# Optimization experiments

Measured on AMD Instinct MI355X. Metric: run time of the kernel, lower is better.

## Reference

```python
import jax, jax.numpy as jnp
import numpy as np

N, E = 50000, 800000
F_IN, HID, HEADS, NCLS = 128, 64, 4, 16
NEG_SLOPE = 0.2


def setup_inputs() -> dict:
    key = jax.random.key(0)
    ks = jax.random.split(key, 16)
    def glorot(k, shape):
        fan_in, fan_out = shape[0], shape[-1]
        lim = jnp.sqrt(6.0 / (fan_in + fan_out))
        return jax.random.uniform(k, shape, jnp.float32, -lim, lim)
    x = jax.random.normal(ks[0], (N, F_IN), jnp.float32)
    edge_index = jax.random.randint(ks[1], (2, E), 0, N, dtype=jnp.int64)
    inp = {"x": x, "edge_index": edge_index}
    # layer 1: F_IN -> HID x HEADS (concat)
    inp["W1"] = glorot(ks[2], (F_IN, HEADS * HID))
    inp["a1_src"] = glorot(ks[3], (HEADS, HID))
    inp["a1_dst"] = glorot(ks[4], (HEADS, HID))
    inp["b1"] = jnp.zeros((HEADS * HID,), jnp.float32)
    # layer 2: HEADS*HID -> HID x HEADS (concat)
    inp["W2"] = glorot(ks[5], (HEADS * HID, HEADS * HID))
    inp["a2_src"] = glorot(ks[6], (HEADS, HID))
    inp["a2_dst"] = glorot(ks[7], (HEADS, HID))
    inp["b2"] = jnp.zeros((HEADS * HID,), jnp.float32)
    # layer 3: HEADS*HID -> NCLS, heads=1, concat=False (mean)
    inp["W3"] = glorot(ks[8], (HEADS * HID, NCLS))
    inp["a3_src"] = glorot(ks[9], (1, NCLS))
    inp["a3_dst"] = glorot(ks[10], (1, NCLS))
    inp["b3"] = jnp.zeros((NCLS,), jnp.float32)
    return inp


def gat_conv(x, src, dst, W, a_src, a_dst, b, heads, out_dim, concat):
    n = x.shape[0]
    h = (x @ W).reshape(n, heads, out_dim)           # [N, H, D]
    s_src = jnp.sum(h * a_src, axis=-1)              # [N, H]
    s_dst = jnp.sum(h * a_dst, axis=-1)              # [N, H]
    e = jax.nn.leaky_relu(s_src[src] + s_dst[dst], NEG_SLOPE)  # [E, H]
    # segment softmax over incoming edges of each dst node
    m = jax.ops.segment_max(e, dst, num_segments=n)
    ex = jnp.exp(e - m[dst])
    z = jax.ops.segment_sum(ex, dst, num_segments=n)
    alpha = ex / z[dst]                              # [E, H]
    msg = h[src] * alpha[:, :, None]                 # [E, H, D]
    out = jax.ops.segment_sum(msg, dst, num_segments=n)  # [N, H, D]
    out = out.reshape(n, heads * out_dim) if concat else out.mean(axis=1)
    return out + b


def reference(x, edge_index, W1, a1_src, a1_dst, b1, W2, a2_src, a2_dst, b2,
              W3, a3_src, a3_dst, b3):
    n = x.shape[0]
    loop = jnp.arange(n, dtype=edge_index.dtype)
    src = jnp.concatenate([edge_index[0], loop])     # add self-loops (PyG default)
    dst = jnp.concatenate([edge_index[1], loop])
    h = jax.nn.elu(gat_conv(x, src, dst, W1, a1_src, a1_dst, b1, HEADS, HID, True))
    h = jax.nn.elu(gat_conv(h, src, dst, W2, a2_src, a2_dst, b2, HEADS, HID, True))
    h = gat_conv(h, src, dst, W3, a3_src, a3_dst, b3, 1, NCLS, False)
    return jax.nn.log_softmax(h, axis=1)
```

## Files before the change

kernel.cpp:

```cpp
#include <hip/hip_runtime.h>
#include <hip/hip_bf16.h>
#include <math.h>

#define N_NODES 50000
#define N_EDGES 800000
#define F_IN    128
#define HID     64
#define HEADS   4
#define NCLS    16
#define NEG_SLOPE 0.2f

typedef __attribute__((ext_vector_type(8))) _Float16 half8v;
typedef __attribute__((ext_vector_type(4))) float f32x4;
typedef __attribute__((ext_vector_type(2))) float f32x2;

static __device__ __forceinline__ float lrelu(float x) {
    return x >= 0.f ? x : NEG_SLOPE * x;
}
static __device__ __forceinline__ unsigned short f2h(float f) {
    _Float16 h = (_Float16)f;
    return __builtin_bit_cast(unsigned short, h);
}
static __device__ __forceinline__ float h2f(unsigned short u) {
    return (float)__builtin_bit_cast(_Float16, u);
}

__global__ void k_zero(int4* __restrict__ p, int n4) {
    int i = blockIdx.x * blockDim.x + threadIdx.x;
    if (i < n4) p[i] = int4{0, 0, 0, 0};
}

#define NB_WT1  128
#define NB_WT2  256
#define NB_HIST 3125
__global__ void k_prep(const float* __restrict__ W1, unsigned short* __restrict__ W1t,
                       const float* __restrict__ W2, unsigned short* __restrict__ W2t,
                       const int* __restrict__ dst, int* __restrict__ counts,
                       unsigned short* __restrict__ rank) {
    int bid = blockIdx.x, tid = threadIdx.x;
    if (bid < NB_WT1) {
        int i = bid * 256 + tid;
        int k = i >> 8, c = i & 255;
        W1t[c * F_IN + k] = f2h(W1[i]);
    } else if (bid < NB_WT1 + NB_WT2) {
        int i = (bid - NB_WT1) * 256 + tid;
        int k = i >> 8, c = i & 255;
        W2t[c * 256 + k] = f2h(W2[i]);
    } else {
        int i = (bid - NB_WT1 - NB_WT2) * 256 + tid;
        if (i < N_EDGES) rank[i] = (unsigned short)atomicAdd(&counts[dst[i]], 1);
    }
}

__global__ __launch_bounds__(256) void k_scan1(const int* __restrict__ counts, int* __restrict__ incl,
                                               int* __restrict__ bsums, int n) {
    __shared__ int wsum[4];
    int blk = blockIdx.x, tid = threadIdx.x;
    int lane = tid & 63, w = tid >> 6;
    int i0 = blk * 1024 + tid * 4;
    int v[4];
    #pragma unroll
    for (int j = 0; j < 4; j++) v[j] = (i0 + j < n) ? counts[i0 + j] : 0;
    int t = v[0] + v[1] + v[2] + v[3];
    int x = t;
    #pragma unroll
    for (int d = 1; d < 64; d <<= 1) { int y = __shfl_up(x, d); if (lane >= d) x += y; }
    if (lane == 63) wsum[w] = x;
    __syncthreads();
    int woff = 0;
    #pragma unroll
    for (int ww = 0; ww < 4; ww++) woff += (ww < w) ? wsum[ww] : 0;
    int p = woff + x - t;
    #pragma unroll
    for (int j = 0; j < 4; j++) { p += v[j]; if (i0 + j < n) incl[i0 + j] = p; }
    if (tid == 255) bsums[blk] = woff + x;
}

__global__ void k_scan2(const int* __restrict__ bsums, int* __restrict__ boffs, int nb, int* rowptr_end) {
    int lane = threadIdx.x;
    int v = (lane < nb) ? bsums[lane] : 0;
    int x = v;
    #pragma unroll
    for (int d = 1; d < 64; d <<= 1) { int y = __shfl_up(x, d); if (lane >= d) x += y; }
    if (lane < nb) boffs[lane] = x - v;
    if (lane == 63) *rowptr_end = x;
}

__global__ void k_scan3(const int* __restrict__ incl, const int* __restrict__ counts,
                        const int* __restrict__ boffs, int* __restrict__ rowptr, int n) {
    int i = blockIdx.x * blockDim.x + threadIdx.x;
    if (i < n) rowptr[i] = boffs[i >> 10] + incl[i] - counts[i];
}

static __device__ __forceinline__ int swz(int r, int lc) {
    return r * 4 + (lc ^ (r & 3) ^ ((r >> 2) & 1));
}

template<int CONVA>
static __device__ __forceinline__ void gemm_body(
        int bid, const void* __restrict__ Av, const unsigned short* __restrict__ Bt,
        const float* __restrict__ asrc, const float* __restrict__ adst,
        unsigned char* __restrict__ C8, float* __restrict__ s_src, float* __restrict__ s_dst,
        int M, int K, unsigned short* Asm, unsigned short* Bsm) {
    int tid = threadIdx.x;
    int lane = tid & 63, wid = tid >> 6;
    int bx = bid & 1, by = bid >> 1;
    int row0 = by * 128, col0 = bx * 128;
    int wr = wid >> 1, wc = wid & 1;
    f32x4 acc[4][4] = {};

    for (int k0 = 0; k0 < K; k0 += 32) {
        __syncthreads();
        #pragma unroll
        for (int s = 0; s < 2; s++) {
            int c = tid + s * 256;
            int row = c >> 2, lc = c & 3;
            int gr = row0 + row; if (gr >= M) gr = 0;
            uint4 va;
            if (CONVA) {
                const float* Af = (const float*)Av + (size_t)gr * K + k0 + lc * 8;
                float4 fa = *(const float4*)Af;
                float4 fb = *(const float4*)(Af + 4);
                va.x = (unsigned)f2h(fa.x) | ((unsigned)f2h(fa.y) << 16);
                va.y = (unsigned)f2h(fa.z) | ((unsigned)f2h(fa.w) << 16);
                va.z = (unsigned)f2h(fb.x) | ((unsigned)f2h(fb.y) << 16);
                va.w = (unsigned)f2h(fb.z) | ((unsigned)f2h(fb.w) << 16);
            } else {
                va = *(const uint4*)((const unsigned short*)Av + (size_t)gr * K + k0 + lc * 8);
            }
            *(uint4*)(&Asm[swz(row, lc) * 8]) = va;
            uint4 vb = *(const uint4*)(Bt + (size_t)(col0 + row) * K + k0 + lc * 8);
            *(uint4*)(&Bsm[swz(row, lc) * 8]) = vb;
        }
        __syncthreads();
        half8v af[4], bg[4];
        int lq = lane >> 4;
        #pragma unroll
        for (int m = 0; m < 4; m++) {
            int r = wr * 64 + m * 16 + (lane & 15);
            af[m] = *(const half8v*)(&Asm[swz(r, lq) * 8]);
        }
        #pragma unroll
        for (int n = 0; n < 4; n++) {
            int r = wc * 64 + n * 16 + (lane & 15);
            bg[n] = *(const half8v*)(&Bsm[swz(r, lq) * 8]);
        }
        #pragma unroll
        for (int m = 0; m < 4; m++)
            #pragma unroll
            for (int n = 0; n < 4; n++)
                acc[m][n] = __builtin_amdgcn_mfma_f32_16x16x32_f16(af[m], bg[n], acc[m][n], 0, 0, 0);
    }

    #pragma unroll
    for (int m = 0; m < 4; m++) {
        #pragma unroll
        for (int r = 0; r < 4; r++) {
            int row = row0 + wr * 64 + m * 16 + (lane >> 4) * 4 + r;
            if (row < M) {
                int q01 = __builtin_amdgcn_cvt_pk_fp8_f32(acc[m][0][r], acc[m][1][r], 0, false);
                int q23 = __builtin_amdgcn_cvt_pk_fp8_f32(acc[m][2][r], acc[m][3][r], 0, false);
                size_t base = (size_t)row * 256 + col0 + wc * 64 + (lane & 15);
                C8[base]      = (unsigned char)(q01 & 0xff);
                C8[base + 16] = (unsigned char)((q01 >> 8) & 0xff);
                C8[base + 32] = (unsigned char)(q23 & 0xff);
                C8[base + 48] = (unsigned char)((q23 >> 8) & 0xff);
            }
        }
    }

    int c16 = lane & 15, lq = lane >> 4;
    int head = bx * 2 + wc;
    float avs[4], avd[4];
    #pragma unroll
    for (int nn = 0; nn < 4; nn++) {
        avs[nn] = asrc[head * 64 + nn * 16 + c16];
        avd[nn] = adst[head * 64 + nn * 16 + c16];
    }
    #pragma unroll
    for (int mm = 0; mm < 4; mm++) {
        #pragma unroll
        for (int r = 0; r < 4; r++) {
            float ps = 0.f, pd = 0.f;
            #pragma unroll
            for (int nn = 0; nn < 4; nn++) {
                ps += acc[mm][nn][r] * avs[nn];
                pd += acc[mm][nn][r] * avd[nn];
            }
            #pragma unroll
            for (int off = 1; off < 16; off <<= 1) {
                ps += __shfl_xor(ps, off);
                pd += __shfl_xor(pd, off);
            }
            if (c16 == 0) {
                int grow = row0 + wr * 64 + mm * 16 + lq * 4 + r;
                if (grow < M) {
                    s_src[grow * 4 + head] = ps;
                    s_dst[grow * 4 + head] = pd;
                }
            }
        }
    }
}

__global__ __launch_bounds__(256) void k_gemm_mfma(const unsigned short* __restrict__ A,
                                                   const unsigned short* __restrict__ Bt,
                                                   const float* __restrict__ asrc,
                                                   const float* __restrict__ adst,
                                                   unsigned char* __restrict__ C8,
                                                   float* __restrict__ s_src,
                                                   float* __restrict__ s_dst,
                                                   int M, int K) {
    __shared__ unsigned short Asm[128 * 32];
    __shared__ unsigned short Bsm[128 * 32];
    gemm_body<0>(blockIdx.x, A, Bt, asrc, adst, C8, s_src, s_dst, M, K, Asm, Bsm);
}

__global__ __launch_bounds__(256) void k_b(const float* __restrict__ A,
                                           const unsigned short* __restrict__ Bt,
                                           const float* __restrict__ asrc,
                                           const float* __restrict__ adst,
                                           unsigned char* __restrict__ C8,
                                           float* __restrict__ s_src,
                                           float* __restrict__ s_dst,
                                           int M, int K, int gemmBlocks,
                                           const int* __restrict__ src, const int* __restrict__ dst,
                                           const int* __restrict__ rowptr,
                                           const unsigned short* __restrict__ rank,
                                           unsigned short* __restrict__ col, int e) {
    __shared__ unsigned short Asm[128 * 32];
    __shared__ unsigned short Bsm[128 * 32];
    int bid = blockIdx.x;
    if (bid < gemmBlocks) {
        gemm_body<1>(bid, A, Bt, asrc, adst, C8, s_src, s_dst, M, K, Asm, Bsm);
    } else {
        int half = (e + 1) >> 1;
        int i = (bid - gemmBlocks) * 256 + (int)threadIdx.x;
        if (i < half) {
            int d = dst[i];
            col[rowptr[d] + rank[i]] = (unsigned short)src[i];
        }
        int j = i + half;
        if (j < e) {
            int d = dst[j];
            col[rowptr[d] + rank[j]] = (unsigned short)src[j];
        }
    }
}

__global__ void k_aggregate(const unsigned char* __restrict__ h8, const int* __restrict__ rowptr,
                            const unsigned short* __restrict__ col,
                            const float* __restrict__ s_src, const float* __restrict__ s_dst,
                            const float* __restrict__ bias,
                            unsigned short* __restrict__ out, int n) {
    int wave = (blockIdx.x * blockDim.x + threadIdx.x) >> 6;
    int lane = threadIdx.x & 63;
    int half = lane >> 5, l5 = lane & 31;
    int node = wave * 2 + half;
    if (node >= n) return;
    int head = l5 >> 3;
    int j8 = l5 & 7;
    int base8 = lane & ~7;
    unsigned foff = (unsigned)(l5 * 8);
    int rs = rowptr[node], re = rowptr[node + 1];
    float sd = s_dst[node * 4 + head];

    float z = 0.f;
    f32x2 a01 = {0.f, 0.f}, a23 = {0.f, 0.f}, a45 = {0.f, 0.f}, a67 = {0.f, 0.f};
    #define PEDGE(SV) __expf(fminf(lrelu((SV) + sd), 80.f))
    #define ACC8(P, HV) { \
        f32x2 pbc = {(P), (P)}; \
        f32x2 v0 = __builtin_amdgcn_cvt_pk_f32_fp8((HV).x, false); \
        f32x2 v1 = __builtin_amdgcn_cvt_pk_f32_fp8((HV).x, true);  \
        f32x2 v2 = __builtin_amdgcn_cvt_pk_f32_fp8((HV).y, false); \
        f32x2 v3 = __builtin_amdgcn_cvt_pk_f32_fp8((HV).y, true);  \
        asm("v_pk_fma_f32 %0, %1, %2, %0" : "+v"(a01) : "v"(v0), "v"(pbc)); \
        asm("v_pk_fma_f32 %0, %1, %2, %0" : "+v"(a23) : "v"(v1), "v"(pbc)); \
        asm("v_pk_fma_f32 %0, %1, %2, %0" : "+v"(a45) : "v"(v2), "v"(pbc)); \
        asm("v_pk_fma_f32 %0, %1, %2, %0" : "+v"(a67) : "v"(v3), "v"(pbc)); \
        z += (P); }

    {
        float pself = PEDGE(s_src[node * 4 + head]);
        uint2 own = *(const uint2*)(h8 + (((unsigned)node << 8) + foff));
        ACC8(pself, own);
    }
    int i = rs;
    for (; i + 7 < re; i += 8) {
        unsigned cc[8];
        #pragma unroll
        for (int j = 0; j < 8; j++) cc[j] = col[i + j];
        float s_own = s_src[cc[j8] * 4 + head];
        uint2 hv[8];
        #pragma unroll
        for (int j = 0; j < 8; j++)
            hv[j] = *(const uint2*)(h8 + ((cc[j] << 8) + foff));
        float p_own = PEDGE(s_own);
        float pv[8];
        #pragma unroll
        for (int j = 0; j < 8; j++) pv[j] = __shfl(p_own, base8 + j);
        #pragma unroll
        for (int j = 0; j < 8; j++) { ACC8(pv[j], hv[j]); }
    }
    for (; i + 3 < re; i += 4) {
        unsigned cc[4];
        #pragma unroll
        for (int j = 0; j < 4; j++) cc[j] = col[i + j];
        float s_own = s_src[cc[j8 & 3] * 4 + head];
        uint2 hv[4];
        #pragma unroll
        for (int j = 0; j < 4; j++)
            hv[j] = *(const uint2*)(h8 + ((cc[j] << 8) + foff));
        float p_own = PEDGE(s_own);
        float pv[4];
        #pragma unroll
        for (int j = 0; j < 4; j++) pv[j] = __shfl(p_own, base8 + j);
        #pragma unroll
        for (int j = 0; j < 4; j++) { ACC8(pv[j], hv[j]); }
    }
    for (; i < re; i++) {
        unsigned c0 = col[i];
        float s0 = s_src[c0 * 4 + head];
        uint2 h0 = *(const uint2*)(h8 + ((c0 << 8) + foff));
        float p0 = PEDGE(s0);
        ACC8(p0, h0);
    }
    #undef ACC8
    #undef PEDGE

    float inv = 1.f / z;
    int f0 = l5 * 8;
    float4 bv0 = *(const float4*)(bias + f0);
    float4 bv1 = *(const float4*)(bias + f0 + 4);
    float o[8];
    o[0] = a01.x * inv + bv0.x; o[1] = a01.y * inv + bv0.y;
    o[2] = a23.x * inv + bv0.z; o[3] = a23.y * inv + bv0.w;
    o[4] = a45.x * inv + bv1.x; o[5] = a45.y * inv + bv1.y;
    o[6] = a67.x * inv + bv1.z; o[7] = a67.y * inv + bv1.w;
    #pragma unroll
    for (int j = 0; j < 8; j++) o[j] = o[j] > 0.f ? o[j] : __expf(o[j]) - 1.f;
    uint4 ov;
    unsigned* w = (unsigned*)&ov;
    #pragma unroll
    for (int j = 0; j < 4; j++)
        w[j] = (unsigned)f2h(o[2 * j]) | ((unsigned)f2h(o[2 * j + 1]) << 16);
    *(uint4*)(out + (size_t)node * 256 + f0) = ov;
}

__global__ __launch_bounds__(256) void k_gemm3(const unsigned short* __restrict__ A,
                                               const float* __restrict__ B,
                                               const float* __restrict__ a3s,
                                               const float* __restrict__ a3d,
                                               unsigned short* __restrict__ C,
                                               float* __restrict__ s_src,
                                               float* __restrict__ s_dst,
                                               int M, int K) {
    __shared__ float Bs[256 * 16];
    for (int i = threadIdx.x; i < K * 16; i += 256) Bs[i] = B[i];
    __syncthreads();
    int tx = threadIdx.x & 15;
    int ty = threadIdx.x >> 4;
    int row = blockIdx.x * 16 + ty;
    if (row >= M) return;
    const unsigned short* Ar = A + (size_t)row * K;
    float acc = 0.f;
    for (int kk = 0; kk < K; kk += 8) {
        uint4 va = *(const uint4*)(Ar + kk);
        const unsigned* u = (const unsigned*)&va;
        #pragma unroll
        for (int j = 0; j < 4; j++) {
            float lo = h2f((unsigned short)(u[j] & 0xffff));
            float hi = h2f((unsigned short)(u[j] >> 16));
            acc += lo * Bs[(kk + 2 * j) * 16 + tx] + hi * Bs[(kk + 2 * j + 1) * 16 + tx];
        }
    }
    C[(size_t)row * 16 + tx] = f2h(acc);
    float ps = acc * a3s[tx], pd = acc * a3d[tx];
    #pragma unroll
    for (int off = 1; off < 16; off <<= 1) {
        ps += __shfl_xor(ps, off);
        pd += __shfl_xor(pd, off);
    }
    if (tx == 0) { s_src[row] = ps; s_dst[row] = pd; }
}

__global__ void k_agg3(const unsigned short* __restrict__ h3, const int* __restrict__ rowptr,
                       const unsigned short* __restrict__ col,
                       const float* __restrict__ s_src, const float* __restrict__ s_dst,
                       const float* __restrict__ b3,
                       float* __restrict__ outp, int n) {
    int wave = (blockIdx.x * blockDim.x + threadIdx.x) >> 6;
    int lane = threadIdx.x & 63;
    if (wave >= n) return;
    int g = lane >> 4, c = lane & 15;
    int gbase = lane & ~15;
    int rs = rowptr[wave], re = rowptr[wave + 1];
    float sdn = s_dst[wave];

    float z = 0.f, acc = 0.f;
    if (g == 0) {
        float p = __expf(fminf(lrelu(s_src[wave] + sdn), 80.f));
        z += p;
        acc += p * h2f(h3[(size_t)wave * 16 + c]);
    }
    int i = rs + g;
    for (; i + 12 < re; i += 16) {
        int ss[4];
        #pragma unroll
        for (int j = 0; j < 4; j++) ss[j] = col[i + 4 * j];
        float q_own = s_src[ss[c & 3]];
        float v0 = h2f(h3[(size_t)ss[0] * 16 + c]), v1 = h2f(h3[(size_t)ss[1] * 16 + c]);
        float v2 = h2f(h3[(size_t)ss[2] * 16 + c]), v3 = h2f(h3[(size_t)ss[3] * 16 + c]);
        float p_own = __expf(fminf(lrelu(q_own + sdn), 80.f));
        float p0 = __shfl(p_own, gbase + 0);
        float p1 = __shfl(p_own, gbase + 1);
        float p2 = __shfl(p_own, gbase + 2);
        float p3 = __shfl(p_own, gbase + 3);
        z += (p0 + p1) + (p2 + p3);
        acc += p0 * v0 + p1 * v1 + p2 * v2 + p3 * v3;
    }
    for (; i < re; i += 4) {
        int s = col[i];
        float p = __expf(fminf(lrelu(s_src[s] + sdn), 80.f));
        z += p;
        acc += p * h2f(h3[(size_t)s * 16 + c]);
    }
    z += __shfl_xor(z, 16);  z += __shfl_xor(z, 32);
    acc += __shfl_xor(acc, 16); acc += __shfl_xor(acc, 32);
    if (lane < 16) {
        float v = acc / z + b3[c];
        float mm = v;
        #pragma unroll
        for (int off = 1; off < 16; off <<= 1) mm = fmaxf(mm, __shfl_xor(mm, off));
        float se = __expf(v - mm);
        #pragma unroll
        for (int off = 1; off < 16; off <<= 1) se += __shfl_xor(se, off);
        outp[(size_t)wave * 16 + c] = v - mm - logf(se);
    }
}

extern "C" void kernel_launch(void* const* d_in, const int* in_sizes, int n_in,
                              void* d_out, int out_size, void* d_ws, size_t ws_size,
                              hipStream_t stream) {
    const float* x      = (const float*)d_in[0];
    const int*   ei     = (const int*)d_in[1];
    const float* W1     = (const float*)d_in[2];
    const float* a1_src = (const float*)d_in[3];
    const float* a1_dst = (const float*)d_in[4];
    const float* b1     = (const float*)d_in[5];
    const float* W2     = (const float*)d_in[6];
    const float* a2_src = (const float*)d_in[7];
    const float* a2_dst = (const float*)d_in[8];
    const float* b2     = (const float*)d_in[9];
    const float* W3     = (const float*)d_in[10];
    const float* a3_src = (const float*)d_in[11];
    const float* a3_dst = (const float*)d_in[12];
    const float* b3     = (const float*)d_in[13];
    float* outp = (float*)d_out;

    const int N = N_NODES, E = N_EDGES;
    const int* src = ei;
    const int* dst = ei + E;

    char* ws = (char*)d_ws;
    size_t off = 0;
    auto alloc = [&](size_t bytes) {
        void* p = ws + off;
        off = (off + bytes + 255) & ~(size_t)255;
        return p;
    };
    int*   rowptr = (int*)alloc((N + 1) * sizeof(int));
    int*   counts = (int*)alloc(N * sizeof(int));
    unsigned short* col = (unsigned short*)alloc(E * sizeof(short));
    unsigned short* rank = (unsigned short*)alloc(E * sizeof(short));
    int*   incl   = (int*)alloc(N * sizeof(int));
    int*   bsums  = (int*)alloc(64 * sizeof(int));
    int*   boffs  = (int*)alloc(64 * sizeof(int));
    float* s_src  = (float*)alloc((size_t)N * HEADS * sizeof(float));
    float* s_dst  = (float*)alloc((size_t)N * HEADS * sizeof(float));
    unsigned short* W1t = (unsigned short*)alloc((size_t)256 * F_IN * sizeof(short));
    unsigned short* W2t = (unsigned short*)alloc((size_t)256 * 256 * sizeof(short));
    unsigned char* hA8  = (unsigned char*)alloc((size_t)N * 256);
    unsigned short* hB  = (unsigned short*)alloc((size_t)N * 256 * sizeof(short));
    unsigned short* h3  = (unsigned short*)alloc((size_t)N * 16 * sizeof(short));
    (void)ws_size;

    const int aggBlocks  = (N + 3) / 4;
    const int aggBlocks2 = (N + 7) / 8;
    const int gemmBlocks = ((N + 127) / 128) * 2;
    const int scatBlocks = ((E + 1) / 2 + 255) / 256;

    k_zero<<<(N / 4 + 255) / 256, 256, 0, stream>>>((int4*)counts, N / 4);
    k_prep<<<NB_WT1 + NB_WT2 + NB_HIST, 256, 0, stream>>>(W1, W1t, W2, W2t, dst, counts, rank);

    const int nb = (N + 1023) / 1024;
    k_scan1<<<nb, 256, 0, stream>>>(counts, incl, bsums, N);
    k_scan2<<<1, 64, 0, stream>>>(bsums, boffs, nb, rowptr + N);
    k_scan3<<<(N + 255) / 256, 256, 0, stream>>>(incl, counts, boffs, rowptr, N);

    k_b<<<gemmBlocks + scatBlocks, 256, 0, stream>>>(x, W1t, a1_src, a1_dst, hA8, s_src, s_dst,
                                                     N, F_IN, gemmBlocks,
                                                     src, dst, rowptr, rank, col, E);
    k_aggregate<<<aggBlocks2, 256, 0, stream>>>(hA8, rowptr, col, s_src, s_dst, b1, hB, N);
    k_gemm_mfma<<<gemmBlocks, 256, 0, stream>>>(hB, W2t, a2_src, a2_dst, hA8, s_src, s_dst, N, 256);
    k_aggregate<<<aggBlocks2, 256, 0, stream>>>(hA8, rowptr, col, s_src, s_dst, b2, hB, N);
    k_gemm3<<<(N + 15) / 16, 256, 0, stream>>>(hB, W3, a3_src, a3_dst, h3, s_src, s_dst, N, 256);
    k_agg3<<<aggBlocks, 256, 0, stream>>>(h3, rowptr, col, s_src, s_dst, b3, outp, N);
}
```

Before: 222.1 us.

## Store fp8 features in 32-column planes and aggregate per plane chunk

The GEMM epilogue now writes fp8 hidden features into eight column-major planes of 32 bytes per node instead of 256-byte rows. The aggregation kernel is reorganized so each block handles one 32-feature chunk for 64 nodes, with 4 lanes per node. The goal is a smaller gather working set per pass so it stays resident in cache. The cost is that each edge's index and score lookups are now repeated across 8 chunks. Layer 3 attention scores move to separate buffers so they no longer overwrite the layer-2 s_src/s_dst, which chunked blocks may still be reading.

```diff
diff --git a/kernel.cpp b/kernel.cpp
--- a/kernel.cpp
+++ b/kernel.cpp
@@ -108,6 +108,7 @@
     int row0 = by * 128, col0 = bx * 128;
     int wr = wid >> 1, wc = wid & 1;
     f32x4 acc[4][4] = {};
+    size_t plane = (size_t)M * 32;
 
     for (int k0 = 0; k0 < K; k0 += 32) {
         __syncthreads();
@@ -160,11 +161,15 @@
             if (row < M) {
                 int q01 = __builtin_amdgcn_cvt_pk_fp8_f32(acc[m][0][r], acc[m][1][r], 0, false);
                 int q23 = __builtin_amdgcn_cvt_pk_fp8_f32(acc[m][2][r], acc[m][3][r], 0, false);
-                size_t base = (size_t)row * 256 + col0 + wc * 64 + (lane & 15);
-                C8[base]      = (unsigned char)(q01 & 0xff);
-                C8[base + 16] = (unsigned char)((q01 >> 8) & 0xff);
-                C8[base + 32] = (unsigned char)(q23 & 0xff);
-                C8[base + 48] = (unsigned char)((q23 >> 8) & 0xff);
+                int f0 = col0 + wc * 64 + (lane & 15);
+                unsigned char b0 = (unsigned char)(q01 & 0xff);
+                unsigned char b1 = (unsigned char)((q01 >> 8) & 0xff);
+                unsigned char b2 = (unsigned char)(q23 & 0xff);
+                unsigned char b3 = (unsigned char)((q23 >> 8) & 0xff);
+                C8[(size_t)((f0) >> 5) * plane + (size_t)row * 32 + ((f0) & 31)]           = b0;
+                C8[(size_t)((f0 + 16) >> 5) * plane + (size_t)row * 32 + ((f0 + 16) & 31)] = b1;
+                C8[(size_t)((f0 + 32) >> 5) * plane + (size_t)row * 32 + ((f0 + 32) & 31)] = b2;
+                C8[(size_t)((f0 + 48) >> 5) * plane + (size_t)row * 32 + ((f0 + 48) & 31)] = b3;
             }
         }
     }
@@ -248,41 +253,44 @@
     }
 }
 
-__global__ void k_aggregate(const unsigned char* __restrict__ h8, const int* __restrict__ rowptr,
-                            const unsigned short* __restrict__ col,
-                            const float* __restrict__ s_src, const float* __restrict__ s_dst,
-                            const float* __restrict__ bias,
-                            unsigned short* __restrict__ out, int n) {
-    int wave = (blockIdx.x * blockDim.x + threadIdx.x) >> 6;
-    int lane = threadIdx.x & 63;
-    int half = lane >> 5, l5 = lane & 31;
-    int node = wave * 2 + half;
+#define PEDGE(SV, SD) __expf(fminf(lrelu((SV) + (SD)), 80.f))
+#define ACC8(P, HV) { \
+    f32x2 pbc = {(P), (P)}; \
+    f32x2 v0 = __builtin_amdgcn_cvt_pk_f32_fp8((HV).x, false); \
+    f32x2 v1 = __builtin_amdgcn_cvt_pk_f32_fp8((HV).x, true);  \
+    f32x2 v2 = __builtin_amdgcn_cvt_pk_f32_fp8((HV).y, false); \
+    f32x2 v3 = __builtin_amdgcn_cvt_pk_f32_fp8((HV).y, true);  \
+    asm("v_pk_fma_f32 %0, %1, %2, %0" : "+v"(a01) : "v"(v0), "v"(pbc)); \
+    asm("v_pk_fma_f32 %0, %1, %2, %0" : "+v"(a23) : "v"(v1), "v"(pbc)); \
+    asm("v_pk_fma_f32 %0, %1, %2, %0" : "+v"(a45) : "v"(v2), "v"(pbc)); \
+    asm("v_pk_fma_f32 %0, %1, %2, %0" : "+v"(a67) : "v"(v3), "v"(pbc)); \
+    z += (P); }
+
+__global__ __launch_bounds__(256) void k_aggc(
+        const unsigned char* __restrict__ h8c,
+        const int* __restrict__ rowptr, const unsigned short* __restrict__ col,
+        const float* __restrict__ s_src, const float* __restrict__ s_dst,
+        const float* __restrict__ bias,
+        unsigned short* __restrict__ out, int n) {
+    int tid = threadIdx.x;
+    int chunk = blockIdx.x & 7;
+    int nb = blockIdx.x >> 3;
+    int lane = tid & 63, wv = tid >> 6;
+    int grp = lane >> 2, lane4 = lane & 3;
+    int node = nb * 64 + wv * 16 + grp;
     if (node >= n) return;
-    int head = l5 >> 3;
-    int j8 = l5 & 7;
-    int base8 = lane & ~7;
-    unsigned foff = (unsigned)(l5 * 8);
+    int head = chunk >> 1;
+    const unsigned char* plane = h8c + (size_t)chunk * n * 32;
+    unsigned foff = (unsigned)(lane4 * 8);
+    int base4 = lane & ~3;
     int rs = rowptr[node], re = rowptr[node + 1];
     float sd = s_dst[node * 4 + head];
 
     float z = 0.f;
     f32x2 a01 = {0.f, 0.f}, a23 = {0.f, 0.f}, a45 = {0.f, 0.f}, a67 = {0.f, 0.f};
-    #define PEDGE(SV) __expf(fminf(lrelu((SV) + sd), 80.f))
-    #define ACC8(P, HV) { \
-        f32x2 pbc = {(P), (P)}; \
-        f32x2 v0 = __builtin_amdgcn_cvt_pk_f32_fp8((HV).x, false); \
-        f32x2 v1 = __builtin_amdgcn_cvt_pk_f32_fp8((HV).x, true);  \
-        f32x2 v2 = __builtin_amdgcn_cvt_pk_f32_fp8((HV).y, false); \
-        f32x2 v3 = __builtin_amdgcn_cvt_pk_f32_fp8((HV).y, true);  \
-        asm("v_pk_fma_f32 %0, %1, %2, %0" : "+v"(a01) : "v"(v0), "v"(pbc)); \
-        asm("v_pk_fma_f32 %0, %1, %2, %0" : "+v"(a23) : "v"(v1), "v"(pbc)); \
-        asm("v_pk_fma_f32 %0, %1, %2, %0" : "+v"(a45) : "v"(v2), "v"(pbc)); \
-        asm("v_pk_fma_f32 %0, %1, %2, %0" : "+v"(a67) : "v"(v3), "v"(pbc)); \
-        z += (P); }
-
     {
-        float pself = PEDGE(s_src[node * 4 + head]);
-        uint2 own = *(const uint2*)(h8 + (((unsigned)node << 8) + foff));
+        float pself = PEDGE(s_src[node * 4 + head], sd);
+        uint2 own = *(const uint2*)(plane + (unsigned)node * 32 + foff);
         ACC8(pself, own);
     }
     int i = rs;
@@ -290,15 +298,20 @@
         unsigned cc[8];
         #pragma unroll
         for (int j = 0; j < 8; j++) cc[j] = col[i + j];
-        float s_own = s_src[cc[j8] * 4 + head];
+        float s0 = s_src[cc[lane4] * 4 + head];
+        float s1 = s_src[cc[4 + lane4] * 4 + head];
         uint2 hv[8];
         #pragma unroll
         for (int j = 0; j < 8; j++)
-            hv[j] = *(const uint2*)(h8 + ((cc[j] << 8) + foff));
-        float p_own = PEDGE(s_own);
+            hv[j] = *(const uint2*)(plane + cc[j] * 32 + foff);
+        float p0o = PEDGE(s0, sd);
+        float p1o = PEDGE(s1, sd);
         float pv[8];
         #pragma unroll
-        for (int j = 0; j < 8; j++) pv[j] = __shfl(p_own, base8 + j);
+        for (int j = 0; j < 4; j++) {
+            pv[j]     = __shfl(p0o, base4 + j);
+            pv[4 + j] = __shfl(p1o, base4 + j);
+        }
         #pragma unroll
         for (int j = 0; j < 8; j++) { ACC8(pv[j], hv[j]); }
     }
@@ -306,30 +319,27 @@
         unsigned cc[4];
         #pragma unroll
         for (int j = 0; j < 4; j++) cc[j] = col[i + j];
-        float s_own = s_src[cc[j8 & 3] * 4 + head];
+        float s0 = s_src[cc[lane4] * 4 + head];
         uint2 hv[4];
         #pragma unroll
         for (int j = 0; j < 4; j++)
-            hv[j] = *(const uint2*)(h8 + ((cc[j] << 8) + foff));
-        float p_own = PEDGE(s_own);
+            hv[j] = *(const uint2*)(plane + cc[j] * 32 + foff);
+        float p0o = PEDGE(s0, sd);
         float pv[4];
         #pragma unroll
-        for (int j = 0; j < 4; j++) pv[j] = __shfl(p_own, base8 + j);
+        for (int j = 0; j < 4; j++) pv[j] = __shfl(p0o, base4 + j);
         #pragma unroll
         for (int j = 0; j < 4; j++) { ACC8(pv[j], hv[j]); }
     }
     for (; i < re; i++) {
         unsigned c0 = col[i];
-        float s0 = s_src[c0 * 4 + head];
-        uint2 h0 = *(const uint2*)(h8 + ((c0 << 8) + foff));
-        float p0 = PEDGE(s0);
+        float p0 = PEDGE(s_src[c0 * 4 + head], sd);
+        uint2 h0 = *(const uint2*)(plane + c0 * 32 + foff);
         ACC8(p0, h0);
     }
-    #undef ACC8
-    #undef PEDGE
 
     float inv = 1.f / z;
-    int f0 = l5 * 8;
+    int f0 = chunk * 32 + lane4 * 8;
     float4 bv0 = *(const float4*)(bias + f0);
     float4 bv1 = *(const float4*)(bias + f0 + 4);
     float o[8];
@@ -340,10 +350,10 @@
     #pragma unroll
     for (int j = 0; j < 8; j++) o[j] = o[j] > 0.f ? o[j] : __expf(o[j]) - 1.f;
     uint4 ov;
-    unsigned* w = (unsigned*)&ov;
+    unsigned* wd = (unsigned*)&ov;
     #pragma unroll
     for (int j = 0; j < 4; j++)
-        w[j] = (unsigned)f2h(o[2 * j]) | ((unsigned)f2h(o[2 * j + 1]) << 16);
+        wd[j] = (unsigned)f2h(o[2 * j]) | ((unsigned)f2h(o[2 * j + 1]) << 16);
     *(uint4*)(out + (size_t)node * 256 + f0) = ov;
 }
 
@@ -478,15 +488,17 @@
     int*   boffs  = (int*)alloc(64 * sizeof(int));
     float* s_src  = (float*)alloc((size_t)N * HEADS * sizeof(float));
     float* s_dst  = (float*)alloc((size_t)N * HEADS * sizeof(float));
+    float* s_src3 = (float*)alloc((size_t)N * sizeof(float));
+    float* s_dst3 = (float*)alloc((size_t)N * sizeof(float));
     unsigned short* W1t = (unsigned short*)alloc((size_t)256 * F_IN * sizeof(short));
     unsigned short* W2t = (unsigned short*)alloc((size_t)256 * 256 * sizeof(short));
-    unsigned char* hA8  = (unsigned char*)alloc((size_t)N * 256);
-    unsigned short* hB  = (unsigned short*)alloc((size_t)N * 256 * sizeof(short));
+    unsigned char* h8c  = (unsigned char*)alloc((size_t)N * 256);
+    unsigned short* hF  = (unsigned short*)alloc((size_t)N * 256 * sizeof(short));
     unsigned short* h3  = (unsigned short*)alloc((size_t)N * 16 * sizeof(short));
     (void)ws_size;
 
     const int aggBlocks  = (N + 3) / 4;
-    const int aggBlocks2 = (N + 7) / 8;
+    const int aggcBlocks = ((N + 63) / 64) * 8;
     const int gemmBlocks = ((N + 127) / 128) * 2;
     const int scatBlocks = ((E + 1) / 2 + 255) / 256;
 
@@ -498,12 +510,12 @@
     k_scan2<<<1, 64, 0, stream>>>(bsums, boffs, nb, rowptr + N);
     k_scan3<<<(N + 255) / 256, 256, 0, stream>>>(incl, counts, boffs, rowptr, N);
 
-    k_b<<<gemmBlocks + scatBlocks, 256, 0, stream>>>(x, W1t, a1_src, a1_dst, hA8, s_src, s_dst,
+    k_b<<<gemmBlocks + scatBlocks, 256, 0, stream>>>(x, W1t, a1_src, a1_dst, h8c, s_src, s_dst,
                                                      N, F_IN, gemmBlocks,
                                                      src, dst, rowptr, rank, col, E);
-    k_aggregate<<<aggBlocks2, 256, 0, stream>>>(hA8, rowptr, col, s_src, s_dst, b1, hB, N);
-    k_gemm_mfma<<<gemmBlocks, 256, 0, stream>>>(hB, W2t, a2_src, a2_dst, hA8, s_src, s_dst, N, 256);
-    k_aggregate<<<aggBlocks2, 256, 0, stream>>>(hA8, rowptr, col, s_src, s_dst, b2, hB, N);
-    k_gemm3<<<(N + 15) / 16, 256, 0, stream>>>(hB, W3, a3_src, a3_dst, h3, s_src, s_dst, N, 256);
-    k_agg3<<<aggBlocks, 256, 0, stream>>>(h3, rowptr, col, s_src, s_dst, b3, outp, N);
-}
+    k_aggc<<<aggcBlocks, 256, 0, stream>>>(h8c, rowptr, col, s_src, s_dst, b1, hF, N);
+    k_gemm_mfma<<<gemmBlocks, 256, 0, stream>>>(hF, W2t, a2_src, a2_dst, h8c, s_src, s_dst, N, 256);
+    k_aggc<<<aggcBlocks, 256, 0, stream>>>(h8c, rowptr, col, s_src, s_dst, b2, hF, N);
+    k_gemm3<<<(N + 15) / 16, 256, 0, stream>>>(hF, W3, a3_src, a3_dst, h3, s_src3, s_dst3, N, 256);
+    k_agg3<<<aggBlocks, 256, 0, stream>>>(h3, rowptr, col, s_src3, s_dst3, b3, outp, N);
+}
```

New measurement: 269.2 us. 1.21x slower.
